# Performance work log

Hardware: AMD Instinct MI355X
Metric: run time of the kernel (lower is better)

The kernel has to match this reference:

```python
import jax, jax.numpy as jnp
import numpy as np

T, B, E, H = 2048, 2, 2048, 16
HD = E // H
SCALE = HD ** -0.5
NEG = -1e9  # large-negative additive mask (finite, safe in fp32/bf16)


def setup_inputs() -> dict:
    key = jax.random.key(0)
    ks = jax.random.split(key, 6)
    query = jax.random.normal(ks[0], (T, B, E), dtype=jnp.float32)
    # causal additive mask, as metaseq builds for decoder self-attention
    attn_mask = jnp.where(jnp.tril(jnp.ones((T, T), dtype=bool)), 0.0, NEG).astype(jnp.float32)
    # combined qkv projection: rows ordered [K | V | Q] per split_tensor_along_last_dim
    qkv_w = jax.random.normal(ks[1], (3 * E, E), dtype=jnp.float32) * (1.0 / np.sqrt(2 * E))
    qkv_b = jax.random.uniform(ks[2], (3 * E,), dtype=jnp.float32, minval=-1, maxval=1) / np.sqrt(E)
    out_w = jax.random.normal(ks[3], (E, E), dtype=jnp.float32) * (1.0 / np.sqrt(2 * E))
    out_b = jax.random.uniform(ks[4], (E,), dtype=jnp.float32, minval=-1, maxval=1) / np.sqrt(E)
    return {"query": query, "attn_mask": attn_mask, "qkv_w": qkv_w,
            "qkv_b": qkv_b, "out_w": out_w, "out_b": out_b}


def reference(query, attn_mask, qkv_w, qkv_b, out_w, out_b):
    t, b, e = query.shape
    # fused QKV projection (ColumnParallelLinear, world_size=1)
    kvq = jnp.einsum('tbe,fe->tbf', query, qkv_w) + qkv_b  # [T,B,3E]
    k, v, q = kvq[..., :e], kvq[..., e:2 * e], kvq[..., 2 * e:]
    q = q * SCALE
    q = q.reshape(t, b, H, HD)
    k = k.reshape(t, b, H, HD)
    v = v.reshape(t, b, H, HD)
    # explicit QK^T bmm -> [B,H,T,S]
    scores = jnp.einsum('tbhd,sbhd->bhts', q, k) + attn_mask[None, None]
    probs = jax.nn.softmax(scores, axis=-1)  # dropout p=0 -> identity
    ctx = jnp.einsum('bhts,sbhd->tbhd', probs, v).reshape(t, b, e)
    # RowParallelLinear out_proj (skip_bias_add in the original; bias added here)
    out = jnp.einsum('tbe,fe->tbf', ctx, out_w) + out_b
    return out
```

## Files before the change

kernel.cpp:

```cpp
#include <hip/hip_runtime.h>
#include <hip/hip_bf16.h>
#include <stdint.h>

#define T_DIM 2048
#define B_DIM 2
#define E_DIM 2048
#define H_DIM 16
#define HD_DIM 128
#define F_DIM 6144
#define ROWS 4096
#define KVB 64

#define QK_SCALE 0.08838834764831845f
#define LOG2E    1.4426950408889634f
#define RESCALE_THR 8.0f

typedef __bf16 bf16_t;
typedef __bf16 bf16x8 __attribute__((ext_vector_type(8)));
typedef __bf16 bf16x4 __attribute__((ext_vector_type(4)));
typedef float  f32x4  __attribute__((ext_vector_type(4)));

__device__ __forceinline__ void gll16(const void* g, void* l) {
  __builtin_amdgcn_global_load_lds((const __attribute__((address_space(1))) void*)g,
                                   (__attribute__((address_space(3))) void*)l, 16, 0, 0);
}

__global__ void cvt_f32_bf16(const float* __restrict__ src, bf16_t* __restrict__ dst, int n4) {
  int i = blockIdx.x * blockDim.x + threadIdx.x;
  int stride = gridDim.x * blockDim.x;
  for (; i < n4; i += stride) {
    float4 v = ((const float4*)src)[i];
    bf16x4 o;
    o[0] = (bf16_t)v.x; o[1] = (bf16_t)v.y; o[2] = (bf16_t)v.z; o[3] = (bf16_t)v.w;
    ((bf16x4*)dst)[i] = o;
  }
}

template<int EPI>
__launch_bounds__(256, 2)
__global__ void gemm_bt(const bf16_t* __restrict__ A, const bf16_t* __restrict__ Bm,
                        const float* __restrict__ bias, void* __restrict__ Cout,
                        int N, int K, int nbn, float qscale, int qcol0)
{
  __shared__ __align__(16) bf16_t As[128][64];
  __shared__ __align__(16) bf16_t Bs[128][64];

  int bid = blockIdx.x;
  int nwg = gridDim.x;
  int cpx = nwg >> 3;
  int swz = (bid & 7) * cpx + (bid >> 3);
  int bm = swz / nbn, bn = swz % nbn;

  int tid = threadIdx.x;
  int lane = tid & 63, wid = tid >> 6;
  int lr = lane & 15, lg = lane >> 4;
  int wm = wid >> 1, wn = wid & 1;

  f32x4 acc[4][4] = {};

  int srow8 = tid >> 3;
  int schunk = tid & 7;

  const bf16_t* gA = A + (size_t)(bm * 128) * K;
  const bf16_t* gB = Bm + (size_t)(bn * 128) * K;

  for (int k0 = 0; k0 < K; k0 += 64) {
    #pragma unroll
    for (int i = 0; i < 4; ++i) {
      int row = i * 32 + srow8;
      int sc = schunk ^ (row & 7);
      gll16(gA + (size_t)row * K + k0 + sc * 8, &As[row][schunk * 8]);
    }
    #pragma unroll
    for (int i = 0; i < 4; ++i) {
      int row = i * 32 + srow8;
      int sc = schunk ^ (row & 7);
      gll16(gB + (size_t)row * K + k0 + sc * 8, &Bs[row][schunk * 8]);
    }
    __syncthreads();

    #pragma unroll
    for (int kk = 0; kk < 2; ++kk) {
      bf16x8 af[4], bfr[4];
      #pragma unroll
      for (int mi = 0; mi < 4; ++mi) {
        int row = wm * 64 + mi * 16 + lr;
        int ch = (kk * 4 + lg) ^ (row & 7);
        af[mi] = *(const bf16x8*)&As[row][ch * 8];
      }
      #pragma unroll
      for (int ni = 0; ni < 4; ++ni) {
        int row = wn * 64 + ni * 16 + lr;
        int ch = (kk * 4 + lg) ^ (row & 7);
        bfr[ni] = *(const bf16x8*)&Bs[row][ch * 8];
      }
      #pragma unroll
      for (int mi = 0; mi < 4; ++mi)
        #pragma unroll
        for (int ni = 0; ni < 4; ++ni)
          acc[mi][ni] = __builtin_amdgcn_mfma_f32_16x16x32_bf16(af[mi], bfr[ni], acc[mi][ni], 0, 0, 0);
    }
    __syncthreads();
  }

  #pragma unroll
  for (int mi = 0; mi < 4; ++mi) {
    int row0 = bm * 128 + wm * 64 + mi * 16 + lg * 4;
    #pragma unroll
    for (int ni = 0; ni < 4; ++ni) {
      int col = bn * 128 + wn * 64 + ni * 16 + lr;
      float bv = bias[col];
      float scl = (EPI == 0 && col >= qcol0) ? qscale : 1.0f;
      #pragma unroll
      for (int r = 0; r < 4; ++r) {
        float v = (acc[mi][ni][r] + bv) * scl;
        if (EPI == 0) ((bf16_t*)Cout)[(size_t)(row0 + r) * N + col] = (bf16_t)v;
        else          ((float*)Cout)[(size_t)(row0 + r) * N + col] = v;
      }
    }
  }
}

__global__ void repack_vt(const bf16_t* __restrict__ KVQ, bf16_t* __restrict__ VTg)
{
  __shared__ __align__(16) bf16_t tile[64][136];
  int bid = blockIdx.x;
  int st = bid & 31, bh = bid >> 5;
  int b = bh >> 4, h = bh & 15;
  int s0 = st * 64;
  int tid = threadIdx.x;

  const bf16_t* vbase = KVQ + (size_t)b * F_DIM + E_DIM + (size_t)h * HD_DIM;
  #pragma unroll
  for (int i = 0; i < 4; ++i) {
    int row = i * 16 + (tid >> 4), c = tid & 15;
    bf16x8 v = *(const bf16x8*)(vbase + (size_t)(s0 + row) * B_DIM * F_DIM + c * 8);
    *(bf16x8*)&tile[row][c * 8] = v;
  }
  __syncthreads();
  bf16_t* out = VTg + (size_t)bh * HD_DIM * T_DIM;
  #pragma unroll
  for (int i = 0; i < 4; ++i) {
    int d = i * 32 + (tid >> 3), c = tid & 7;
    bf16x8 o;
    #pragma unroll
    for (int j = 0; j < 8; ++j) o[j] = tile[c * 8 + j][d];
    *(bf16x8*)(out + (size_t)d * T_DIM + s0 + c * 8) = o;
  }
}

__launch_bounds__(256, 2)
__global__ void attn3(const bf16_t* __restrict__ KVQ, const bf16_t* __restrict__ VTg,
                      bf16_t* __restrict__ CTX)
{
  __shared__ __align__(16) bf16_t Ks[2][KVB][128];
  __shared__ __align__(16) bf16_t Vs[2][128][KVB];
  __shared__ __align__(16) bf16_t Ps[4][32 * 64];

  int bid = blockIdx.x;
  int xcd = bid & 7;
  int j   = bid >> 3;
  int hi  = j >> 5;
  int mid = (j >> 4) & 1;
  int q   = j & 15;
  int bh  = xcd * 4 + hi * 2 + mid;
  int qt  = hi ? (15 - q) : q;
  int b = bh >> 4, h = bh & 15;

  int tid = threadIdx.x;
  int lane = tid & 63, wid = tid >> 6;
  int lr = lane & 15, lg = lane >> 4;

  const bf16_t* kbase = KVQ + (size_t)b * F_DIM + (size_t)h * HD_DIM;
  const bf16_t* vtb   = VTg + (size_t)bh * HD_DIM * T_DIM;
  bf16_t* PsW = &Ps[wid][0];

  bf16x8 qf[2][4];
  #pragma unroll
  for (int mf = 0; mf < 2; ++mf) {
    int t = qt * 128 + wid * 32 + mf * 16 + lr;
    const bf16_t* qb = KVQ + ((size_t)t * B_DIM + b) * F_DIM + 2 * E_DIM + h * HD_DIM;
    #pragma unroll
    for (int ks = 0; ks < 4; ++ks) qf[mf][ks] = *(const bf16x8*)(qb + ks * 32 + lg * 8);
  }

  f32x4 ctxa[2][8] = {};
  float m[2][4], lsum[2][4];
  #pragma unroll
  for (int mf = 0; mf < 2; ++mf)
    #pragma unroll
    for (int r = 0; r < 4; ++r) { m[mf][r] = -1e30f; lsum[mf][r] = 0.0f; }

  int krow = tid >> 4, kch = tid & 15;
  int vrow = tid >> 3, vch = tid & 7;

  auto stage = [&](int buf, int it) {
    int s0 = it * KVB;
    #pragma unroll
    for (int i = 0; i < 4; ++i) {
      int row = i * 16 + krow;
      int sc = kch ^ (row & 7);
      gll16(kbase + (size_t)(s0 + row) * B_DIM * F_DIM + sc * 8, &Ks[buf][row][kch * 8]);
    }
    #pragma unroll
    for (int i = 0; i < 4; ++i) {
      int row = i * 32 + vrow;
      int sc = vch ^ (row & 7);
      gll16(vtb + (size_t)row * T_DIM + s0 + sc * 8, &Vs[buf][row][vch * 8]);
    }
  };

  int nt = 2 * (qt + 1);
  stage(0, 0);
  __syncthreads();

  int tqw = qt * 128 + wid * 32;

  for (int it = 0; it < nt; ++it) {
    int cur = it & 1;
    if (it + 1 < nt) stage(cur ^ 1, it + 1);
    int s0 = it * KVB;
    bool diag = (it >= nt - 2);

    f32x4 sacc[2][4] = {};
    __builtin_amdgcn_s_setprio(1);
    #pragma unroll
    for (int ks = 0; ks < 4; ++ks) {
      #pragma unroll
      for (int nti = 0; nti < 4; ++nti) {
        int srow = nti * 16 + lr;
        int slot = (ks * 4 + lg) ^ (srow & 7);
        bf16x8 kf = *(const bf16x8*)&Ks[cur][srow][slot * 8];
        sacc[0][nti] = __builtin_amdgcn_mfma_f32_16x16x32_bf16(qf[0][ks], kf, sacc[0][nti], 0, 0, 0);
        sacc[1][nti] = __builtin_amdgcn_mfma_f32_16x16x32_bf16(qf[1][ks], kf, sacc[1][nti], 0, 0, 0);
      }
    }
    __builtin_amdgcn_s_setprio(0);

    float mxl = -1e30f;
    #pragma unroll
    for (int mf = 0; mf < 2; ++mf)
      #pragma unroll
      for (int r = 0; r < 4; ++r)
        #pragma unroll
        for (int nti = 0; nti < 4; ++nti) {
          float v = sacc[mf][nti][r];
          if (diag) v = (s0 + nti * 16 + lr > tqw + mf * 16 + lg * 4 + r) ? -1e30f : v;
          sacc[mf][nti][r] = v;
          mxl = fmaxf(mxl, v - m[mf][r]);
        }
    if (!__all(mxl <= RESCALE_THR)) {
      #pragma unroll
      for (int mf = 0; mf < 2; ++mf)
        #pragma unroll
        for (int r = 0; r < 4; ++r) {
          float mx = fmaxf(fmaxf(sacc[mf][0][r], sacc[mf][1][r]),
                           fmaxf(sacc[mf][2][r], sacc[mf][3][r]));
          #pragma unroll
          for (int d = 1; d < 16; d <<= 1) mx = fmaxf(mx, __shfl_xor(mx, d, 64));
          float mn = fmaxf(m[mf][r], mx);
          float rs = exp2f(m[mf][r] - mn);
          m[mf][r] = mn;
          lsum[mf][r] *= rs;
          #pragma unroll
          for (int dt = 0; dt < 8; ++dt) ctxa[mf][dt][r] *= rs;
        }
    }
    #pragma unroll
    for (int mf = 0; mf < 2; ++mf)
      #pragma unroll
      for (int r = 0; r < 4; ++r) {
        int prow = mf * 16 + lg * 4 + r;
        #pragma unroll
        for (int nti = 0; nti < 4; ++nti) {
          float p = exp2f(sacc[mf][nti][r] - m[mf][r]);
          lsum[mf][r] += p;
          int chk = (nti * 2 + (lr >> 3)) ^ (prow & 7);
          PsW[prow * 64 + chk * 8 + (lr & 7)] = (bf16_t)p;
        }
      }
    asm volatile("s_waitcnt lgkmcnt(0)" ::: "memory");
    __builtin_amdgcn_sched_barrier(0);

    bf16x8 pf[2][2];
    #pragma unroll
    for (int mf = 0; mf < 2; ++mf) {
      int prow = mf * 16 + lr;
      #pragma unroll
      for (int kh = 0; kh < 2; ++kh) {
        int chk = (kh * 4 + lg) ^ (prow & 7);
        pf[mf][kh] = *(const bf16x8*)&PsW[prow * 64 + chk * 8];
      }
    }
    __builtin_amdgcn_s_setprio(1);
    #pragma unroll
    for (int dt = 0; dt < 8; ++dt) {
      int drow = dt * 16 + lr;
      int sl0 = lg ^ (drow & 7);
      int sl1 = (4 + lg) ^ (drow & 7);
      bf16x8 vf0 = *(const bf16x8*)&Vs[cur][drow][sl0 * 8];
      bf16x8 vf1 = *(const bf16x8*)&Vs[cur][drow][sl1 * 8];
      ctxa[0][dt] = __builtin_amdgcn_mfma_f32_16x16x32_bf16(pf[0][0], vf0, ctxa[0][dt], 0, 0, 0);
      ctxa[0][dt] = __builtin_amdgcn_mfma_f32_16x16x32_bf16(pf[0][1], vf1, ctxa[0][dt], 0, 0, 0);
      ctxa[1][dt] = __builtin_amdgcn_mfma_f32_16x16x32_bf16(pf[1][0], vf0, ctxa[1][dt], 0, 0, 0);
      ctxa[1][dt] = __builtin_amdgcn_mfma_f32_16x16x32_bf16(pf[1][1], vf1, ctxa[1][dt], 0, 0, 0);
    }
    __builtin_amdgcn_s_setprio(0);

    __syncthreads();
  }

  #pragma unroll
  for (int mf = 0; mf < 2; ++mf)
    #pragma unroll
    for (int r = 0; r < 4; ++r) {
      #pragma unroll
      for (int d = 1; d < 16; d <<= 1) lsum[mf][r] += __shfl_xor(lsum[mf][r], d, 64);
    }

  #pragma unroll
  for (int mf = 0; mf < 2; ++mf)
    #pragma unroll
    for (int r = 0; r < 4; ++r) {
      int t = qt * 128 + wid * 32 + mf * 16 + lg * 4 + r;
      float inv = 1.0f / lsum[mf][r];
      bf16_t* out = CTX + ((size_t)t * B_DIM + b) * E_DIM + h * HD_DIM;
      #pragma unroll
      for (int dt = 0; dt < 8; ++dt)
        out[dt * 16 + lr] = (bf16_t)(ctxa[mf][dt][r] * inv);
    }
}

extern "C" void kernel_launch(void* const* d_in, const int* in_sizes, int n_in,
                              void* d_out, int out_size, void* d_ws, size_t ws_size,
                              hipStream_t stream)
{
  const float* query = (const float*)d_in[0];
  const float* qkv_w = (const float*)d_in[2];
  const float* qkv_b = (const float*)d_in[3];
  const float* out_w = (const float*)d_in[4];
  const float* out_b = (const float*)d_in[5];

  bf16_t* Xbf  = (bf16_t*)d_ws;
  bf16_t* Wqkv = Xbf  + (size_t)ROWS * E_DIM;
  bf16_t* Wout = Wqkv + (size_t)F_DIM * E_DIM;
  bf16_t* KVQ  = Wout + (size_t)E_DIM * E_DIM;
  bf16_t* CTX  = Xbf;
  bf16_t* VTg  = Wqkv;

  cvt_f32_bf16<<<2048, 256, 0, stream>>>(query, Xbf,  ROWS * E_DIM / 4);
  cvt_f32_bf16<<<2048, 256, 0, stream>>>(qkv_w, Wqkv, F_DIM * E_DIM / 4);
  cvt_f32_bf16<<<2048, 256, 0, stream>>>(out_w, Wout, E_DIM * E_DIM / 4);

  gemm_bt<0><<<32 * 48, 256, 0, stream>>>(Xbf, Wqkv, qkv_b, KVQ,
                                          F_DIM, E_DIM, 48, QK_SCALE * LOG2E, 2 * E_DIM);

  repack_vt<<<32 * 32, 256, 0, stream>>>(KVQ, VTg);

  attn3<<<512, 256, 0, stream>>>(KVQ, VTg, CTX);

  gemm_bt<1><<<32 * 16, 256, 0, stream>>>(CTX, Wout, out_b, (float*)d_out,
                                          E_DIM, E_DIM, 16, 1.0f, 1 << 30);
}
```

Before: 281.7 us.

## Fuse V transpose into QKV GEMM epilogue and merge conversion kernels

The QKV GEMM epilogue now writes V tiles transposed through shared memory straight into the VT buffer. K and Q go to a compacted 4096-wide buffer, so the separate repack_vt kernel and the round trip of V through global memory are gone. The three fp32-to-bf16 conversion launches are merged into one kernel. This saves two launches and some memory traffic, at the cost of a more complex epilogue and an extra block-level sync in the V blocks.

```diff
diff --git a/kernel.cpp b/kernel.cpp
--- a/kernel.cpp
+++ b/kernel.cpp
@@ -8,6 +8,7 @@
 #define H_DIM 16
 #define HD_DIM 128
 #define F_DIM 6144
+#define F2   4096
 #define ROWS 4096
 #define KVB 64
 
@@ -25,29 +26,35 @@
                                    (__attribute__((address_space(3))) void*)l, 16, 0, 0);
 }
 
-__global__ void cvt_f32_bf16(const float* __restrict__ src, bf16_t* __restrict__ dst, int n4) {
+__global__ void cvt3(const float* __restrict__ s0, bf16_t* __restrict__ d0, int n0,
+                     const float* __restrict__ s1, bf16_t* __restrict__ d1, int n1,
+                     const float* __restrict__ s2, bf16_t* __restrict__ d2, int n2) {
+  int total = n0 + n1 + n2;
   int i = blockIdx.x * blockDim.x + threadIdx.x;
   int stride = gridDim.x * blockDim.x;
-  for (; i < n4; i += stride) {
-    float4 v = ((const float4*)src)[i];
+  for (; i < total; i += stride) {
+    const float* s; bf16_t* d; int j;
+    if (i < n0)            { s = s0; d = d0; j = i; }
+    else if (i < n0 + n1)  { s = s1; d = d1; j = i - n0; }
+    else                   { s = s2; d = d2; j = i - n0 - n1; }
+    float4 v = ((const float4*)s)[j];
     bf16x4 o;
     o[0] = (bf16_t)v.x; o[1] = (bf16_t)v.y; o[2] = (bf16_t)v.z; o[3] = (bf16_t)v.w;
-    ((bf16x4*)dst)[i] = o;
-  }
-}
-
-template<int EPI>
+    ((bf16x4*)d)[j] = o;
+  }
+}
+
 __launch_bounds__(256, 2)
-__global__ void gemm_bt(const bf16_t* __restrict__ A, const bf16_t* __restrict__ Bm,
-                        const float* __restrict__ bias, void* __restrict__ Cout,
-                        int N, int K, int nbn, float qscale, int qcol0)
+__global__ void gemm_qkv(const bf16_t* __restrict__ A, const bf16_t* __restrict__ Bm,
+                         const float* __restrict__ bias, bf16_t* __restrict__ KVQ2,
+                         bf16_t* __restrict__ VTg)
 {
-  __shared__ __align__(16) bf16_t As[128][64];
-  __shared__ __align__(16) bf16_t Bs[128][64];
+  __shared__ __align__(16) bf16_t Sm[2][128][64];
+  bf16_t* Tp = &Sm[0][0][0];
+  const int K = E_DIM, nbn = 48;
 
   int bid = blockIdx.x;
-  int nwg = gridDim.x;
-  int cpx = nwg >> 3;
+  int cpx = gridDim.x >> 3;
   int swz = (bid & 7) * cpx + (bid >> 3);
   int bm = swz / nbn, bn = swz % nbn;
 
@@ -69,6 +76,126 @@
     for (int i = 0; i < 4; ++i) {
       int row = i * 32 + srow8;
       int sc = schunk ^ (row & 7);
+      gll16(gA + (size_t)row * K + k0 + sc * 8, &Sm[0][row][schunk * 8]);
+    }
+    #pragma unroll
+    for (int i = 0; i < 4; ++i) {
+      int row = i * 32 + srow8;
+      int sc = schunk ^ (row & 7);
+      gll16(gB + (size_t)row * K + k0 + sc * 8, &Sm[1][row][schunk * 8]);
+    }
+    __syncthreads();
+
+    #pragma unroll
+    for (int kk = 0; kk < 2; ++kk) {
+      bf16x8 af[4], bfr[4];
+      #pragma unroll
+      for (int mi = 0; mi < 4; ++mi) {
+        int row = wm * 64 + mi * 16 + lr;
+        int ch = (kk * 4 + lg) ^ (row & 7);
+        af[mi] = *(const bf16x8*)&Sm[0][row][ch * 8];
+      }
+      #pragma unroll
+      for (int ni = 0; ni < 4; ++ni) {
+        int row = wn * 64 + ni * 16 + lr;
+        int ch = (kk * 4 + lg) ^ (row & 7);
+        bfr[ni] = *(const bf16x8*)&Sm[1][row][ch * 8];
+      }
+      #pragma unroll
+      for (int mi = 0; mi < 4; ++mi)
+        #pragma unroll
+        for (int ni = 0; ni < 4; ++ni)
+          acc[mi][ni] = __builtin_amdgcn_mfma_f32_16x16x32_bf16(af[mi], bfr[ni], acc[mi][ni], 0, 0, 0);
+    }
+    __syncthreads();
+  }
+
+  if (bn >= 16 && bn < 32) {
+    int h = bn - 16;
+    #pragma unroll
+    for (int mi = 0; mi < 4; ++mi) {
+      int row0 = wm * 64 + mi * 16 + lg * 4;
+      #pragma unroll
+      for (int ni = 0; ni < 4; ++ni) {
+        int lc = wn * 64 + ni * 16 + lr;
+        float bv = bias[bn * 128 + lc];
+        bf16x4 pk;
+        #pragma unroll
+        for (int r = 0; r < 4; ++r) pk[r] = (bf16_t)(acc[mi][ni][r] + bv);
+        int rowX = row0 ^ ((lc & 15) << 3);
+        *(bf16x4*)&Tp[lc * 128 + rowX] = pk;
+      }
+    }
+    __syncthreads();
+    int d = tid >> 1, half = tid & 1;
+    int sz = (d & 15) << 3;
+    size_t tb = (size_t)bm * 64 + half * 32;
+    bf16_t* o0 = VTg + ((size_t)h        * 128 + d) * T_DIM + tb;
+    bf16_t* o1 = VTg + ((size_t)(16 + h) * 128 + d) * T_DIM + tb;
+    #pragma unroll
+    for (int kk = 0; kk < 4; ++kk) {
+      int rl = half * 64 + kk * 16;
+      bf16x8 v0 = *(const bf16x8*)&Tp[d * 128 + ((rl)     ^ sz)];
+      bf16x8 v1 = *(const bf16x8*)&Tp[d * 128 + ((rl + 8) ^ sz)];
+      bf16x8 ev, od;
+      #pragma unroll
+      for (int j = 0; j < 4; ++j) {
+        ev[j] = v0[2 * j];     ev[4 + j] = v1[2 * j];
+        od[j] = v0[2 * j + 1]; od[4 + j] = v1[2 * j + 1];
+      }
+      *(bf16x8*)(o0 + kk * 8) = ev;
+      *(bf16x8*)(o1 + kk * 8) = od;
+    }
+  } else {
+    bool isQ = (bn >= 32);
+    float scl = isQ ? (QK_SCALE * LOG2E) : 1.0f;
+    int colOff = isQ ? -2048 : 0;
+    #pragma unroll
+    for (int mi = 0; mi < 4; ++mi) {
+      int row0 = bm * 128 + wm * 64 + mi * 16 + lg * 4;
+      #pragma unroll
+      for (int ni = 0; ni < 4; ++ni) {
+        int col = bn * 128 + wn * 64 + ni * 16 + lr;
+        float bv = bias[col];
+        #pragma unroll
+        for (int r = 0; r < 4; ++r) {
+          float v = (acc[mi][ni][r] + bv) * scl;
+          KVQ2[(size_t)(row0 + r) * F2 + col + colOff] = (bf16_t)v;
+        }
+      }
+    }
+  }
+}
+
+__launch_bounds__(256, 2)
+__global__ void gemm_out(const bf16_t* __restrict__ A, const bf16_t* __restrict__ Bm,
+                         const float* __restrict__ bias, float* __restrict__ Cout)
+{
+  __shared__ __align__(16) bf16_t As[128][64];
+  __shared__ __align__(16) bf16_t Bs[128][64];
+  const int K = E_DIM, N = E_DIM, nbn = 16;
+
+  int bid = blockIdx.x;
+  int cpx = gridDim.x >> 3;
+  int swz = (bid & 7) * cpx + (bid >> 3);
+  int bm = swz / nbn, bn = swz % nbn;
+
+  int tid = threadIdx.x;
+  int lane = tid & 63, wid = tid >> 6;
+  int lr = lane & 15, lg = lane >> 4;
+  int wm = wid >> 1, wn = wid & 1;
+
+  f32x4 acc[4][4] = {};
+  int srow8 = tid >> 3, schunk = tid & 7;
+
+  const bf16_t* gA = A + (size_t)(bm * 128) * K;
+  const bf16_t* gB = Bm + (size_t)(bn * 128) * K;
+
+  for (int k0 = 0; k0 < K; k0 += 64) {
+    #pragma unroll
+    for (int i = 0; i < 4; ++i) {
+      int row = i * 32 + srow8;
+      int sc = schunk ^ (row & 7);
       gll16(gA + (size_t)row * K + k0 + sc * 8, &As[row][schunk * 8]);
     }
     #pragma unroll
@@ -110,47 +237,15 @@
     for (int ni = 0; ni < 4; ++ni) {
       int col = bn * 128 + wn * 64 + ni * 16 + lr;
       float bv = bias[col];
-      float scl = (EPI == 0 && col >= qcol0) ? qscale : 1.0f;
-      #pragma unroll
-      for (int r = 0; r < 4; ++r) {
-        float v = (acc[mi][ni][r] + bv) * scl;
-        if (EPI == 0) ((bf16_t*)Cout)[(size_t)(row0 + r) * N + col] = (bf16_t)v;
-        else          ((float*)Cout)[(size_t)(row0 + r) * N + col] = v;
-      }
-    }
-  }
-}
-
-__global__ void repack_vt(const bf16_t* __restrict__ KVQ, bf16_t* __restrict__ VTg)
-{
-  __shared__ __align__(16) bf16_t tile[64][136];
-  int bid = blockIdx.x;
-  int st = bid & 31, bh = bid >> 5;
-  int b = bh >> 4, h = bh & 15;
-  int s0 = st * 64;
-  int tid = threadIdx.x;
-
-  const bf16_t* vbase = KVQ + (size_t)b * F_DIM + E_DIM + (size_t)h * HD_DIM;
-  #pragma unroll
-  for (int i = 0; i < 4; ++i) {
-    int row = i * 16 + (tid >> 4), c = tid & 15;
-    bf16x8 v = *(const bf16x8*)(vbase + (size_t)(s0 + row) * B_DIM * F_DIM + c * 8);
-    *(bf16x8*)&tile[row][c * 8] = v;
-  }
-  __syncthreads();
-  bf16_t* out = VTg + (size_t)bh * HD_DIM * T_DIM;
-  #pragma unroll
-  for (int i = 0; i < 4; ++i) {
-    int d = i * 32 + (tid >> 3), c = tid & 7;
-    bf16x8 o;
-    #pragma unroll
-    for (int j = 0; j < 8; ++j) o[j] = tile[c * 8 + j][d];
-    *(bf16x8*)(out + (size_t)d * T_DIM + s0 + c * 8) = o;
+      #pragma unroll
+      for (int r = 0; r < 4; ++r)
+        Cout[(size_t)(row0 + r) * N + col] = acc[mi][ni][r] + bv;
+    }
   }
 }
 
 __launch_bounds__(256, 2)
-__global__ void attn3(const bf16_t* __restrict__ KVQ, const bf16_t* __restrict__ VTg,
+__global__ void attn3(const bf16_t* __restrict__ KVQ2, const bf16_t* __restrict__ VTg,
                       bf16_t* __restrict__ CTX)
 {
   __shared__ __align__(16) bf16_t Ks[2][KVB][128];
@@ -171,7 +266,7 @@
   int lane = tid & 63, wid = tid >> 6;
   int lr = lane & 15, lg = lane >> 4;
 
-  const bf16_t* kbase = KVQ + (size_t)b * F_DIM + (size_t)h * HD_DIM;
+  const bf16_t* kbase = KVQ2 + (size_t)b * F2 + (size_t)h * HD_DIM;
   const bf16_t* vtb   = VTg + (size_t)bh * HD_DIM * T_DIM;
   bf16_t* PsW = &Ps[wid][0];
 
@@ -179,7 +274,7 @@
   #pragma unroll
   for (int mf = 0; mf < 2; ++mf) {
     int t = qt * 128 + wid * 32 + mf * 16 + lr;
-    const bf16_t* qb = KVQ + ((size_t)t * B_DIM + b) * F_DIM + 2 * E_DIM + h * HD_DIM;
+    const bf16_t* qb = KVQ2 + ((size_t)t * B_DIM + b) * F2 + E_DIM + h * HD_DIM;
     #pragma unroll
     for (int ks = 0; ks < 4; ++ks) qf[mf][ks] = *(const bf16x8*)(qb + ks * 32 + lg * 8);
   }
@@ -200,7 +295,7 @@
     for (int i = 0; i < 4; ++i) {
       int row = i * 16 + krow;
       int sc = kch ^ (row & 7);
-      gll16(kbase + (size_t)(s0 + row) * B_DIM * F_DIM + sc * 8, &Ks[buf][row][kch * 8]);
+      gll16(kbase + (size_t)(s0 + row) * B_DIM * F2 + sc * 8, &Ks[buf][row][kch * 8]);
     }
     #pragma unroll
     for (int i = 0; i < 4; ++i) {
@@ -344,21 +439,17 @@
   bf16_t* Xbf  = (bf16_t*)d_ws;
   bf16_t* Wqkv = Xbf  + (size_t)ROWS * E_DIM;
   bf16_t* Wout = Wqkv + (size_t)F_DIM * E_DIM;
-  bf16_t* KVQ  = Wout + (size_t)E_DIM * E_DIM;
+  bf16_t* KVQ2 = Wout + (size_t)E_DIM * E_DIM;
+  bf16_t* VTg  = KVQ2 + (size_t)ROWS * F2;
   bf16_t* CTX  = Xbf;
-  bf16_t* VTg  = Wqkv;
-
-  cvt_f32_bf16<<<2048, 256, 0, stream>>>(query, Xbf,  ROWS * E_DIM / 4);
-  cvt_f32_bf16<<<2048, 256, 0, stream>>>(qkv_w, Wqkv, F_DIM * E_DIM / 4);
-  cvt_f32_bf16<<<2048, 256, 0, stream>>>(out_w, Wout, E_DIM * E_DIM / 4);
-
-  gemm_bt<0><<<32 * 48, 256, 0, stream>>>(Xbf, Wqkv, qkv_b, KVQ,
-                                          F_DIM, E_DIM, 48, QK_SCALE * LOG2E, 2 * E_DIM);
-
-  repack_vt<<<32 * 32, 256, 0, stream>>>(KVQ, VTg);
-
-  attn3<<<512, 256, 0, stream>>>(KVQ, VTg, CTX);
-
-  gemm_bt<1><<<32 * 16, 256, 0, stream>>>(CTX, Wout, out_b, (float*)d_out,
-                                          E_DIM, E_DIM, 16, 1.0f, 1 << 30);
-}
+
+  cvt3<<<2048, 256, 0, stream>>>(query, Xbf,  ROWS * E_DIM / 4,
+                                 qkv_w, Wqkv, F_DIM * E_DIM / 4,
+                                 out_w, Wout, E_DIM * E_DIM / 4);
+
+  gemm_qkv<<<32 * 48, 256, 0, stream>>>(Xbf, Wqkv, qkv_b, KVQ2, VTg);
+
+  attn3<<<512, 256, 0, stream>>>(KVQ2, VTg, CTX);
+
+  gemm_out<<<32 * 16, 256, 0, stream>>>(CTX, Wout, out_b, (float*)d_out);
+}
```

Result: faster. 269.9 us (-4.2%).
